# Optimization experiments

Measured on AMD Instinct MI355X. Metric: run time of the kernel, lower is better.

## Reference

```python
import jax, jax.numpy as jnp
import numpy as np

NUM_LEVELS = 8
BASE_H = 512
BASE_W = 512
CHANNELS = 16
N_QUERIES = 1000000


def _resize_bilinear(tex, h, w):
    """PyTorch F.interpolate(mode='bilinear', align_corners=False). tex: (C,H,W) -> (C,h,w)."""
    C, H, W = tex.shape

    def coords(out_size, in_size):
        # half-pixel source coords, clamped at 0 like PyTorch
        src = (jnp.arange(out_size, dtype=jnp.float32) + 0.5) * (in_size / out_size) - 0.5
        src = jnp.maximum(src, 0.0)
        i0 = jnp.minimum(jnp.floor(src).astype(jnp.int32), in_size - 1)
        i1 = jnp.minimum(i0 + 1, in_size - 1)
        t = src - i0.astype(jnp.float32)
        return i0, i1, t

    y0, y1, ty = coords(h, H)
    x0, x1, tx = coords(w, W)
    rows = tex[:, y0, :] * (1.0 - ty)[None, :, None] + tex[:, y1, :] * ty[None, :, None]  # (C,h,W)
    out = rows[:, :, x0] * (1.0 - tx) + rows[:, :, x1] * tx  # (C,h,w)
    return out


def _grid_sample(tex, gx, gy):
    """PyTorch F.grid_sample(mode='bilinear', padding_mode='border', align_corners=True).
    tex: (C,h,w); gx,gy: (N,) in [-1,1]. Returns (N,C)."""
    C, h, w = tex.shape
    x = jnp.clip((gx + 1.0) * 0.5 * (w - 1), 0.0, w - 1)
    y = jnp.clip((gy + 1.0) * 0.5 * (h - 1), 0.0, h - 1)
    x0 = jnp.clip(jnp.floor(x).astype(jnp.int32), 0, w - 1)
    y0 = jnp.clip(jnp.floor(y).astype(jnp.int32), 0, h - 1)
    x1 = jnp.minimum(x0 + 1, w - 1)
    y1 = jnp.minimum(y0 + 1, h - 1)
    fx = x - x0.astype(x.dtype)
    fy = y - y0.astype(y.dtype)
    v00 = tex[:, y0, x0]  # (C,N)
    v01 = tex[:, y0, x1]
    v10 = tex[:, y1, x0]
    v11 = tex[:, y1, x1]
    out = (v00 * (1 - fx) * (1 - fy) + v01 * fx * (1 - fy)
           + v10 * (1 - fx) * fy + v11 * fx * fy)  # (C,N)
    return out.T  # (N,C)


def setup_inputs() -> dict:
    key = jax.random.key(0)
    k1, k2, k3 = jax.random.split(key, 3)
    uv = jax.random.uniform(k1, (N_QUERIES, 2), dtype=jnp.float32)
    p = jax.random.uniform(k2, (N_QUERIES,), dtype=jnp.float32)
    tex = jax.random.normal(k3, (1, CHANNELS, BASE_H, BASE_W), dtype=jnp.float32) * 0.01
    return {"uv": uv, "p": p, "tex": tex}


def reference(uv, p, tex):
    tex2 = tex[0]  # (C,H,W)
    gx = 2.0 * uv[:, 0] - 1.0
    gy = 2.0 * uv[:, 1] - 1.0
    levels = []
    for i in range(NUM_LEVELS):
        h = max(BASE_H >> i, 1)
        w = max(BASE_W >> i, 1)
        t = _resize_bilinear(tex2, h, w)
        levels.append(_grid_sample(t, gx, gy))  # (N,C)
    big = jnp.stack(levels, axis=1)  # (N,L,C)
    lf = p * (NUM_LEVELS - 1)
    l0 = jnp.floor(lf).astype(jnp.int32)
    l1 = jnp.minimum(l0 + 1, NUM_LEVELS - 1)
    alpha = (lf - l0.astype(lf.dtype))[:, None]  # (N,1)
    out0 = jnp.take_along_axis(big, l0[:, None, None], axis=1)[:, 0]  # (N,C)
    out1 = jnp.take_along_axis(big, l1[:, None, None], axis=1)[:, 0]
    return out0 * (1.0 - alpha) + out1 * alpha
```

## Files before the change

kernel.cpp:

```cpp
#include <hip/hip_runtime.h>

static constexpr int BASE = 512;

__constant__ int d_off[8] = {0, 4194304, 5242880, 5505024, 5570560, 5586944, 5591040, 5592064};

__global__ void transpose_l0(const float* __restrict__ tex, float* __restrict__ dst) {
    int pix = blockIdx.x * blockDim.x + threadIdx.x;
    float v[16];
#pragma unroll
    for (int c = 0; c < 16; ++c) v[c] = tex[c * 262144 + pix];
    float4* o = (float4*)(dst + (size_t)pix * 16);
    o[0] = make_float4(v[0], v[1], v[2], v[3]);
    o[1] = make_float4(v[4], v[5], v[6], v[7]);
    o[2] = make_float4(v[8], v[9], v[10], v[11]);
    o[3] = make_float4(v[12], v[13], v[14], v[15]);
}

__global__ void build_levels(const float* __restrict__ l0, float* __restrict__ ws) {
    int lev = blockIdx.y + 1;
    int w = BASE >> lev;
    int npix = w * w;
    int pix = blockIdx.x * blockDim.x + threadIdx.x;
    if (pix >= npix) return;
    int y = pix >> (9 - lev);
    int x = pix & (w - 1);
    int xx = (x << lev) + (1 << (lev - 1)) - 1;
    int yy = (y << lev) + (1 << (lev - 1)) - 1;
    const float4* t = (const float4*)l0;
    float4* dst = (float4*)(ws + d_off[lev] + (size_t)pix * 16);
    int i00 = (yy * 512 + xx) * 4;
    int i01 = i00 + 4;
    int i10 = i00 + 512 * 4;
    int i11 = i10 + 4;
#pragma unroll
    for (int q = 0; q < 4; ++q) {
        float4 a = t[i00 + q];
        float4 b = t[i01 + q];
        float4 c = t[i10 + q];
        float4 d = t[i11 + q];
        float4 r;
        r.x = (a.x * 0.5f + c.x * 0.5f) * 0.5f + (b.x * 0.5f + d.x * 0.5f) * 0.5f;
        r.y = (a.y * 0.5f + c.y * 0.5f) * 0.5f + (b.y * 0.5f + d.y * 0.5f) * 0.5f;
        r.z = (a.z * 0.5f + c.z * 0.5f) * 0.5f + (b.z * 0.5f + d.z * 0.5f) * 0.5f;
        r.w = (a.w * 0.5f + c.w * 0.5f) * 0.5f + (b.w * 0.5f + d.w * 0.5f) * 0.5f;
        dst[q] = r;
    }
}

__global__ void sample_kernel(const float* __restrict__ uv, const float* __restrict__ p,
                              const float* __restrict__ ws, float* __restrict__ out, int N) {
    int tid = blockIdx.x * blockDim.x + threadIdx.x;
    int n = tid >> 2;
    int q = tid & 3;
    if (n >= N) return;

    float u0 = uv[2 * n];
    float v0 = uv[2 * n + 1];
    float pp = p[n];
    float gx = 2.0f * u0 - 1.0f;
    float gy = 2.0f * v0 - 1.0f;

    float lf = pp * 7.0f;
    int l0 = (int)floorf(lf);
    l0 = max(0, min(l0, 7));
    int l1 = min(l0 + 1, 7);
    float alpha = lf - (float)l0;

    float4 r[2];
    int ls[2] = {l0, l1};
#pragma unroll
    for (int k = 0; k < 2; ++k) {
        int l = ls[k];
        int w = BASE >> l;
        float wm1 = (float)(w - 1);
        float x = (gx + 1.0f) * 0.5f * wm1;
        x = fminf(fmaxf(x, 0.0f), wm1);
        float y = (gy + 1.0f) * 0.5f * wm1;
        y = fminf(fmaxf(y, 0.0f), wm1);
        int x0 = (int)x;
        int y0 = (int)y;
        x0 = min(x0, w - 1);
        y0 = min(y0, w - 1);
        int x1 = min(x0 + 1, w - 1);
        int y1 = min(y0 + 1, w - 1);
        float fx = x - (float)x0;
        float fy = y - (float)y0;

        const float4* t = (const float4*)(ws + d_off[l]);
        float4 v00 = t[(y0 * w + x0) * 4 + q];
        float4 v01 = t[(y0 * w + x1) * 4 + q];
        float4 v10 = t[(y1 * w + x0) * 4 + q];
        float4 v11 = t[(y1 * w + x1) * 4 + q];

        float w00 = (1.0f - fx) * (1.0f - fy);
        float w01 = fx * (1.0f - fy);
        float w10 = (1.0f - fx) * fy;
        float w11 = fx * fy;
        r[k].x = v00.x * w00 + v01.x * w01 + v10.x * w10 + v11.x * w11;
        r[k].y = v00.y * w00 + v01.y * w01 + v10.y * w10 + v11.y * w11;
        r[k].z = v00.z * w00 + v01.z * w01 + v10.z * w10 + v11.z * w11;
        r[k].w = v00.w * w00 + v01.w * w01 + v10.w * w10 + v11.w * w11;
    }

    float4 o;
    o.x = r[0].x * (1.0f - alpha) + r[1].x * alpha;
    o.y = r[0].y * (1.0f - alpha) + r[1].y * alpha;
    o.z = r[0].z * (1.0f - alpha) + r[1].z * alpha;
    o.w = r[0].w * (1.0f - alpha) + r[1].w * alpha;
    ((float4*)out)[n * 4 + q] = o;
}

extern "C" void kernel_launch(void* const* d_in, const int* in_sizes, int n_in,
                              void* d_out, int out_size, void* d_ws, size_t ws_size,
                              hipStream_t stream) {
    const float* uv  = (const float*)d_in[0];
    const float* p   = (const float*)d_in[1];
    const float* tex = (const float*)d_in[2];
    float* out = (float*)d_out;
    float* ws  = (float*)d_ws;
    int N = in_sizes[1];

    transpose_l0<<<262144 / 256, 256, 0, stream>>>(tex, ws);

    dim3 gA2(256, 7);
    build_levels<<<gA2, 256, 0, stream>>>(ws, ws);

    long long total = (long long)N * 4;
    int blocks = (int)((total + 255) / 256);
    sample_kernel<<<blocks, 256, 0, stream>>>(uv, p, ws, out, N);
}
```

Measured before the change: 150.4 us.

## Store mipmap pyramid in fp16 and sample with two threads per query

The texture pyramid is now stored as half precision, 16 channels in 32 bytes per texel. Each query is handled by two threads that each gather 8 channels with one 16-byte load per corner, instead of four threads each loading 4 floats. The aim is to halve gather bytes and cache footprint for the random texel reads, and to cut per-query index math. The fp16 rounding adds error relative to the fp32 reference, and the texture values (~0.01 scale) sit close to the range where half loses relative precision.

```diff
diff --git a/kernel.cpp b/kernel.cpp
--- a/kernel.cpp
+++ b/kernel.cpp
@@ -1,22 +1,38 @@
 #include <hip/hip_runtime.h>
+#include <hip/hip_fp16.h>
 
 static constexpr int BASE = 512;
 
-__constant__ int d_off[8] = {0, 4194304, 5242880, 5505024, 5570560, 5586944, 5591040, 5592064};
+__constant__ int c_off[8] = {0, 4194304, 5242880, 5505024, 5570560, 5586944, 5591040, 5592064};
 
-__global__ void transpose_l0(const float* __restrict__ tex, float* __restrict__ dst) {
+__global__ void transpose_l0(const float* __restrict__ tex, __half* __restrict__ dst) {
     int pix = blockIdx.x * blockDim.x + threadIdx.x;
     float v[16];
 #pragma unroll
     for (int c = 0; c < 16; ++c) v[c] = tex[c * 262144 + pix];
+    __half2 h[8];
+#pragma unroll
+    for (int i = 0; i < 8; ++i) h[i] = __floats2half2_rn(v[2 * i], v[2 * i + 1]);
     float4* o = (float4*)(dst + (size_t)pix * 16);
-    o[0] = make_float4(v[0], v[1], v[2], v[3]);
-    o[1] = make_float4(v[4], v[5], v[6], v[7]);
-    o[2] = make_float4(v[8], v[9], v[10], v[11]);
-    o[3] = make_float4(v[12], v[13], v[14], v[15]);
+    o[0] = *(const float4*)&h[0];
+    o[1] = *(const float4*)&h[4];
 }
 
-__global__ void build_levels(const float* __restrict__ l0, float* __restrict__ ws) {
+__device__ inline void load_texel16(const __half* p, float* f) {
+    float4 r0 = ((const float4*)p)[0];
+    float4 r1 = ((const float4*)p)[1];
+    const __half2* h0 = (const __half2*)&r0;
+    const __half2* h1 = (const __half2*)&r1;
+#pragma unroll
+    for (int i = 0; i < 4; ++i) {
+        float2 a = __half22float2(h0[i]);
+        f[2 * i] = a.x; f[2 * i + 1] = a.y;
+        float2 b = __half22float2(h1[i]);
+        f[8 + 2 * i] = b.x; f[9 + 2 * i] = b.y;
+    }
+}
+
+__global__ void build_levels(const __half* __restrict__ l0, __half* __restrict__ ws) {
     int lev = blockIdx.y + 1;
     int w = BASE >> lev;
     int npix = w * w;
@@ -26,48 +42,50 @@
     int x = pix & (w - 1);
     int xx = (x << lev) + (1 << (lev - 1)) - 1;
     int yy = (y << lev) + (1 << (lev - 1)) - 1;
-    const float4* t = (const float4*)l0;
-    float4* dst = (float4*)(ws + d_off[lev] + (size_t)pix * 16);
-    int i00 = (yy * 512 + xx) * 4;
-    int i01 = i00 + 4;
-    int i10 = i00 + 512 * 4;
-    int i11 = i10 + 4;
+    const __half* b00 = l0 + (size_t)(yy * 512 + xx) * 16;
+    float a[16], b[16], c[16], d[16];
+    load_texel16(b00, a);
+    load_texel16(b00 + 16, b);
+    load_texel16(b00 + 512 * 16, c);
+    load_texel16(b00 + 512 * 16 + 16, d);
+    __half2 r[8];
 #pragma unroll
-    for (int q = 0; q < 4; ++q) {
-        float4 a = t[i00 + q];
-        float4 b = t[i01 + q];
-        float4 c = t[i10 + q];
-        float4 d = t[i11 + q];
-        float4 r;
-        r.x = (a.x * 0.5f + c.x * 0.5f) * 0.5f + (b.x * 0.5f + d.x * 0.5f) * 0.5f;
-        r.y = (a.y * 0.5f + c.y * 0.5f) * 0.5f + (b.y * 0.5f + d.y * 0.5f) * 0.5f;
-        r.z = (a.z * 0.5f + c.z * 0.5f) * 0.5f + (b.z * 0.5f + d.z * 0.5f) * 0.5f;
-        r.w = (a.w * 0.5f + c.w * 0.5f) * 0.5f + (b.w * 0.5f + d.w * 0.5f) * 0.5f;
-        dst[q] = r;
+    for (int i = 0; i < 8; ++i) {
+        float r0 = (a[2 * i] * 0.5f + c[2 * i] * 0.5f) * 0.5f +
+                   (b[2 * i] * 0.5f + d[2 * i] * 0.5f) * 0.5f;
+        float r1 = (a[2 * i + 1] * 0.5f + c[2 * i + 1] * 0.5f) * 0.5f +
+                   (b[2 * i + 1] * 0.5f + d[2 * i + 1] * 0.5f) * 0.5f;
+        r[i] = __floats2half2_rn(r0, r1);
     }
+    float4* dst = (float4*)(ws + c_off[lev] + (size_t)pix * 16);
+    dst[0] = *(const float4*)&r[0];
+    dst[1] = *(const float4*)&r[4];
 }
 
-__global__ void sample_kernel(const float* __restrict__ uv, const float* __restrict__ p,
-                              const float* __restrict__ ws, float* __restrict__ out, int N) {
+__global__ void sample_kernel(const float2* __restrict__ uv, const float* __restrict__ p,
+                              const __half* __restrict__ ws, float* __restrict__ out, int N) {
     int tid = blockIdx.x * blockDim.x + threadIdx.x;
-    int n = tid >> 2;
-    int q = tid & 3;
+    int n = tid >> 1;
+    int q = tid & 1;
     if (n >= N) return;
 
-    float u0 = uv[2 * n];
-    float v0 = uv[2 * n + 1];
+    float2 uvn = uv[n];
     float pp = p[n];
-    float gx = 2.0f * u0 - 1.0f;
-    float gy = 2.0f * v0 - 1.0f;
+    float gx = 2.0f * uvn.x - 1.0f;
+    float gy = 2.0f * uvn.y - 1.0f;
 
     float lf = pp * 7.0f;
-    int l0 = (int)floorf(lf);
-    l0 = max(0, min(l0, 7));
+    int l0 = (int)lf;
+    l0 = min(l0, 7);
     int l1 = min(l0 + 1, 7);
     float alpha = lf - (float)l0;
 
-    float4 r[2];
+    float acc[8];
+#pragma unroll
+    for (int j = 0; j < 8; ++j) acc[j] = 0.0f;
+
     int ls[2] = {l0, l1};
+    float lw[2] = {1.0f - alpha, alpha};
 #pragma unroll
     for (int k = 0; k < 2; ++k) {
         int l = ls[k];
@@ -77,37 +95,45 @@
         x = fminf(fmaxf(x, 0.0f), wm1);
         float y = (gy + 1.0f) * 0.5f * wm1;
         y = fminf(fmaxf(y, 0.0f), wm1);
-        int x0 = (int)x;
-        int y0 = (int)y;
-        x0 = min(x0, w - 1);
-        y0 = min(y0, w - 1);
+        int x0 = min((int)x, w - 1);
+        int y0 = min((int)y, w - 1);
         int x1 = min(x0 + 1, w - 1);
         int y1 = min(y0 + 1, w - 1);
         float fx = x - (float)x0;
         float fy = y - (float)y0;
 
-        const float4* t = (const float4*)(ws + d_off[l]);
-        float4 v00 = t[(y0 * w + x0) * 4 + q];
-        float4 v01 = t[(y0 * w + x1) * 4 + q];
-        float4 v10 = t[(y1 * w + x0) * 4 + q];
-        float4 v11 = t[(y1 * w + x1) * 4 + q];
+        const __half* t = ws + c_off[l] + 8 * q;
+        float v00[8], v01[8], v10[8], v11[8];
+        {
+            float4 r00 = *(const float4*)(t + (size_t)(y0 * w + x0) * 16);
+            float4 r01 = *(const float4*)(t + (size_t)(y0 * w + x1) * 16);
+            float4 r10 = *(const float4*)(t + (size_t)(y1 * w + x0) * 16);
+            float4 r11 = *(const float4*)(t + (size_t)(y1 * w + x1) * 16);
+            const __half2* h00 = (const __half2*)&r00;
+            const __half2* h01 = (const __half2*)&r01;
+            const __half2* h10 = (const __half2*)&r10;
+            const __half2* h11 = (const __half2*)&r11;
+#pragma unroll
+            for (int i = 0; i < 4; ++i) {
+                float2 a = __half22float2(h00[i]); v00[2 * i] = a.x; v00[2 * i + 1] = a.y;
+                float2 b = __half22float2(h01[i]); v01[2 * i] = b.x; v01[2 * i + 1] = b.y;
+                float2 c = __half22float2(h10[i]); v10[2 * i] = c.x; v10[2 * i + 1] = c.y;
+                float2 d = __half22float2(h11[i]); v11[2 * i] = d.x; v11[2 * i + 1] = d.y;
+            }
+        }
 
-        float w00 = (1.0f - fx) * (1.0f - fy);
-        float w01 = fx * (1.0f - fy);
-        float w10 = (1.0f - fx) * fy;
-        float w11 = fx * fy;
-        r[k].x = v00.x * w00 + v01.x * w01 + v10.x * w10 + v11.x * w11;
-        r[k].y = v00.y * w00 + v01.y * w01 + v10.y * w10 + v11.y * w11;
-        r[k].z = v00.z * w00 + v01.z * w01 + v10.z * w10 + v11.z * w11;
-        r[k].w = v00.w * w00 + v01.w * w01 + v10.w * w10 + v11.w * w11;
+        float w00 = (1.0f - fx) * (1.0f - fy) * lw[k];
+        float w01 = fx * (1.0f - fy) * lw[k];
+        float w10 = (1.0f - fx) * fy * lw[k];
+        float w11 = fx * fy * lw[k];
+#pragma unroll
+        for (int j = 0; j < 8; ++j)
+            acc[j] += v00[j] * w00 + v01[j] * w01 + v10[j] * w10 + v11[j] * w11;
     }
 
-    float4 o;
-    o.x = r[0].x * (1.0f - alpha) + r[1].x * alpha;
-    o.y = r[0].y * (1.0f - alpha) + r[1].y * alpha;
-    o.z = r[0].z * (1.0f - alpha) + r[1].z * alpha;
-    o.w = r[0].w * (1.0f - alpha) + r[1].w * alpha;
-    ((float4*)out)[n * 4 + q] = o;
+    float4* o = (float4*)(out + (size_t)n * 16 + 8 * q);
+    o[0] = make_float4(acc[0], acc[1], acc[2], acc[3]);
+    o[1] = make_float4(acc[4], acc[5], acc[6], acc[7]);
 }
 
 extern "C" void kernel_launch(void* const* d_in, const int* in_sizes, int n_in,
@@ -117,7 +143,7 @@
     const float* p   = (const float*)d_in[1];
     const float* tex = (const float*)d_in[2];
     float* out = (float*)d_out;
-    float* ws  = (float*)d_ws;
+    __half* ws = (__half*)d_ws;
     int N = in_sizes[1];
 
     transpose_l0<<<262144 / 256, 256, 0, stream>>>(tex, ws);
@@ -125,7 +151,7 @@
     dim3 gA2(256, 7);
     build_levels<<<gA2, 256, 0, stream>>>(ws, ws);
 
-    long long total = (long long)N * 4;
+    long long total = (long long)N * 2;
     int blocks = (int)((total + 255) / 256);
-    sample_kernel<<<blocks, 256, 0, stream>>>(uv, p, ws, out, N);
+    sample_kernel<<<blocks, 256, 0, stream>>>((const float2*)uv, p, ws, out, N);
 }
```

Measured after the change: 132.2 us. -12.1%, faster.
